# Performance work log

Measured on AMD Instinct MI355X. Metric: run time of the kernel, lower is better.

Reference implementation:

```python
import jax, jax.numpy as jnp
import numpy as np

ALPHA = 0.2  # LeakyReLU negative slope


def setup_inputs() -> dict:
    key = jax.random.key(0)
    k1, k2, k3 = jax.random.split(key, 3)
    B, N, F_in, F_out = 8, 2048, 256, 256
    h = jax.random.normal(k1, (B, N, F_in), dtype=jnp.float32)
    adj = jax.random.randint(k2, (B, N, N), 0, 2, dtype=jnp.int32)
    # xavier_uniform for W [F_in, F_out]
    limit = float(np.sqrt(6.0 / (F_in + F_out)))
    W = jax.random.uniform(k3, (F_in, F_out), dtype=jnp.float32, minval=-limit, maxval=limit)
    return {"h": h, "adj": adj, "W": W}


def reference(h, adj, W):
    # h: [B,N,F_in], W: [F_in,F_out] -> Wh: [B,N,F_out]
    Wh = jnp.einsum('bnf,fo->bno', h, W)
    # (Wh_i + Wh_j).sum(-1) == s[p] + s[q] with s = Wh.sum(-1); avoids [B,N,N,F] tensor
    s = Wh.sum(axis=-1)  # [B,N]
    e = jax.nn.leaky_relu(s[:, :, None] + s[:, None, :], negative_slope=ALPHA)  # [B,N,N]
    e = jnp.where(adj == 0, -jnp.inf, e)
    alpha = jax.nn.softmax(e, axis=-1)  # masked softmax over neighbors
    # dropout is identity in eval mode
    h_prime = jnp.einsum('bpq,bqo->bpo', alpha, Wh)  # [B,N,F_out]
    return h_prime
```

## Files before the change

kernel.cpp:

```cpp
#include <hip/hip_runtime.h>
#include <hip/hip_bf16.h>
#include <stdint.h>

#define LEAKY_ALPHA 0.2f

using f32x4 = __attribute__((ext_vector_type(4))) float;
using u32x2 = __attribute__((ext_vector_type(2))) unsigned int;
using u32x4 = __attribute__((ext_vector_type(4))) unsigned int;
using i32x4 = __attribute__((ext_vector_type(4))) int;
using s16x8 = __attribute__((ext_vector_type(8))) short;

static __device__ __forceinline__ unsigned short f2bf(float x) {
  __hip_bfloat16 b = __float2bfloat16(x);
  return __builtin_bit_cast(unsigned short, b);
}

__global__ __launch_bounds__(256) void gat_prep(
    const float* __restrict__ W, __hip_bfloat16* __restrict__ WT,
    float* __restrict__ wsum)
{
  const int o = blockIdx.x;
  const int t = threadIdx.x;
  WT[o * 256 + t] = __float2bfloat16(W[t * 256 + o]);
  float u = W[o * 256 + t];
#pragma unroll
  for (int off = 1; off < 64; off <<= 1) u += __shfl_xor(u, off, 64);
  __shared__ float red[4];
  if ((t & 63) == 0) red[t >> 6] = u;
  __syncthreads();
  if (t == 0) wsum[o] = red[0] + red[1] + red[2] + red[3];
}

__global__ __launch_bounds__(256) void gat_wh2(
    const float* __restrict__ h, const __hip_bfloat16* __restrict__ WT,
    const float* __restrict__ wsum, __hip_bfloat16* __restrict__ WhT,
    float* __restrict__ s)
{
  const int b = blockIdx.x >> 5;
  const int q0 = (blockIdx.x & 31) * 64;
  const int t = threadIdx.x;
  const int wid = t >> 6, lane = t & 63;

  __shared__ __align__(16) unsigned char Bh[64 * 512];
  __shared__ __align__(16) unsigned char Aw[256 * 128];
  __shared__ __align__(16) float wsl[256];

  wsl[t] = wsum[t];
  __syncthreads();

  {
    const int q = t >> 2;
    const int fs = (t & 3) * 64;
    const float* hrow = h + ((size_t)(b * 2048 + q0 + q)) * 256 + fs;
    float sp = 0.f;
#pragma unroll
    for (int c = 0; c < 8; ++c) {
      const f32x4 a  = *(const f32x4*)&hrow[c * 8];
      const f32x4 bq = *(const f32x4*)&hrow[c * 8 + 4];
      const f32x4 wa = *(const f32x4*)&wsl[fs + c * 8];
      const f32x4 wb = *(const f32x4*)&wsl[fs + c * 8 + 4];
      sp += a[0]*wa[0] + a[1]*wa[1] + a[2]*wa[2] + a[3]*wa[3]
          + bq[0]*wb[0] + bq[1]*wb[1] + bq[2]*wb[2] + bq[3]*wb[3];
      u32x4 pk;
      pk[0] = (unsigned)f2bf(a[0])  | ((unsigned)f2bf(a[1])  << 16);
      pk[1] = (unsigned)f2bf(a[2])  | ((unsigned)f2bf(a[3])  << 16);
      pk[2] = (unsigned)f2bf(bq[0]) | ((unsigned)f2bf(bq[1]) << 16);
      pk[3] = (unsigned)f2bf(bq[2]) | ((unsigned)f2bf(bq[3]) << 16);
      const int boff = q * 512 + ((fs * 2 + c * 16) ^ ((q & 7) << 4));
      *(u32x4*)&Bh[boff] = pk;
    }
    sp += __shfl_xor(sp, 1, 64);
    sp += __shfl_xor(sp, 2, 64);
    if ((t & 3) == 0) s[b * 2048 + q0 + q] = sp;
  }

  f32x4 acc[4][4];
#pragma unroll
  for (int i = 0; i < 4; ++i)
#pragma unroll
    for (int j = 0; j < 4; ++j) acc[i][j] = (f32x4)(0.f);

  for (int it = 0; it < 4; ++it) {
    const int f0 = it * 64;
    __syncthreads();
#pragma unroll
    for (int j = 0; j < 8; ++j) {
      const int o = (t >> 3) + 32 * j;
      const int c = t & 7;
      const u32x4 v = *(const u32x4*)&WT[o * 256 + f0 + c * 8];
      *(u32x4*)&Aw[o * 128 + ((c * 16) ^ ((o & 7) << 4))] = v;
    }
    __syncthreads();
#pragma unroll
    for (int kt = 0; kt < 2; ++kt) {
      const int kb = kt * 64 + ((lane >> 4) << 4);
      s16x8 af[4], bf[4];
#pragma unroll
      for (int qt = 0; qt < 4; ++qt) {
        const int qr = qt * 16 + (lane & 15);
        af[qt] = *(const s16x8*)&Bh[qr * 512 + ((f0 * 2 + kb) ^ ((qr & 7) << 4))];
      }
#pragma unroll
      for (int ot = 0; ot < 4; ++ot) {
        const int orow = wid * 64 + ot * 16 + (lane & 15);
        bf[ot] = *(const s16x8*)&Aw[orow * 128 + (kb ^ ((orow & 7) << 4))];
      }
#pragma unroll
      for (int qt = 0; qt < 4; ++qt)
#pragma unroll
        for (int ot = 0; ot < 4; ++ot)
          acc[qt][ot] = __builtin_amdgcn_mfma_f32_16x16x32_bf16(
              af[qt], bf[ot], acc[qt][ot], 0, 0, 0);
    }
  }

  __hip_bfloat16* __restrict__ WhTb = WhT + (size_t)b * 256 * 2048;
#pragma unroll
  for (int qt = 0; qt < 4; ++qt)
#pragma unroll
    for (int ot = 0; ot < 4; ++ot) {
      const int o = wid * 64 + ot * 16 + (lane & 15);
      const int ql = q0 + qt * 16 + ((lane >> 4) << 2);
      u32x2 pk;
      pk[0] = (unsigned)f2bf(acc[qt][ot][0]) | ((unsigned)f2bf(acc[qt][ot][1]) << 16);
      pk[1] = (unsigned)f2bf(acc[qt][ot][2]) | ((unsigned)f2bf(acc[qt][ot][3]) << 16);
      *(u32x2*)&WhTb[(size_t)o * 2048 + ql] = pk;
    }
}

__global__ __launch_bounds__(512, 2) void gat_attn(
    const int* __restrict__ adj, const float* __restrict__ s,
    const __hip_bfloat16* __restrict__ WhT, float* __restrict__ out)
{
  const int N = 2048;
  const int bid = blockIdx.x;
  const int swz = (bid & 7) * 32 + (bid >> 3);
  const int b = swz >> 5;
  const int p0 = (swz & 31) * 64;
  const int t = threadIdx.x;
  const int wid = t >> 6, lane = t & 63;

  __shared__ __align__(16) unsigned char Bs[2][256 * 128];
  __shared__ __align__(16) unsigned char Pt[2][64 * 128];
  __shared__ __align__(16) float red_sh[8];
  __shared__ __align__(16) float l_sh[64];

  const int sp_row = t >> 3;
  const int sq8 = (t & 7) * 8;
  const int* __restrict__ adjrow = adj + ((size_t)(b * N + p0 + sp_row)) * N;
  const float* __restrict__ sB = s + b * N;
  const __hip_bfloat16* __restrict__ WhTb = WhT + (size_t)b * 256 * 2048;
  const int ptoff = sp_row * 128 + (((t & 7) ^ (sp_row & 7)) << 4);

  const int grow = t >> 3;
  const int gchunk = t & 7;
  const size_t gsrc_off = (size_t)grow * 2048 + (size_t)((gchunk ^ (grow & 7)) << 3);
  const int ldst = wid * 1024;

  const int pg = wid >> 2;
  const int og = wid & 3;

#pragma unroll
  for (int c = 0; c < 4; ++c)
    __builtin_amdgcn_global_load_lds(
        (const __attribute__((address_space(1))) unsigned int*)(WhTb + gsrc_off + (size_t)c * 64 * 2048),
        (__attribute__((address_space(3))) unsigned int*)&Bs[0][c * 8192 + ldst],
        16, 0, 0);
  i32x4 aE0 = *(const i32x4*)&adjrow[sq8];
  i32x4 aE1 = *(const i32x4*)&adjrow[sq8 + 4];
  f32x4 sE0 = *(const f32x4*)&sB[sq8];
  f32x4 sE1 = *(const f32x4*)&sB[sq8 + 4];
  i32x4 aO0 = *(const i32x4*)&adjrow[64 + sq8];
  i32x4 aO1 = *(const i32x4*)&adjrow[64 + sq8 + 4];
  f32x4 sO0 = *(const f32x4*)&sB[64 + sq8];
  f32x4 sO1 = *(const f32x4*)&sB[64 + sq8 + 4];

  const f32x4 s4 = *(const f32x4*)&sB[t * 4];
  float bm = fmaxf(fmaxf(s4[0], s4[1]), fmaxf(s4[2], s4[3]));
#pragma unroll
  for (int off = 1; off < 64; off <<= 1) bm = fmaxf(bm, __shfl_xor(bm, off, 64));
  if (lane == 0) red_sh[wid] = bm;
  const float s_p = sB[p0 + sp_row];
  __syncthreads();
  float smax = red_sh[0];
#pragma unroll
  for (int k = 1; k < 8; ++k) smax = fmaxf(smax, red_sh[k]);
  const float xm = s_p + smax;
  const float m_p = (xm > 0.f) ? xm : (LEAKY_ALPHA * xm);

  f32x4 acc[2][4];
#pragma unroll
  for (int pt = 0; pt < 2; ++pt)
#pragma unroll
    for (int ot = 0; ot < 4; ++ot) acc[pt][ot] = (f32x4)(0.f);
  float lacc = 0.f;

  auto phase = [&](int BI, int QQ, i32x4& A0, i32x4& A1, f32x4& S0, f32x4& S1)
      __attribute__((always_inline)) {
    float wv[8];
#pragma unroll
    for (int i = 0; i < 4; ++i) {
      const float x = s_p + S0[i];
      const float le = (x > 0.f) ? x : (LEAKY_ALPHA * x);
      const float w = __expf(le - m_p);
      wv[i] = (A0[i] != 0) ? w : 0.f;
      lacc += wv[i];
    }
#pragma unroll
    for (int i = 0; i < 4; ++i) {
      const float x = s_p + S1[i];
      const float le = (x > 0.f) ? x : (LEAKY_ALPHA * x);
      const float w = __expf(le - m_p);
      wv[4 + i] = (A1[i] != 0) ? w : 0.f;
      lacc += wv[4 + i];
    }
    {
      u32x4 pw;
#pragma unroll
      for (int k2 = 0; k2 < 4; ++k2)
        pw[k2] = (unsigned)f2bf(wv[2 * k2]) |
                 ((unsigned)f2bf(wv[2 * k2 + 1]) << 16);
      *(u32x4*)&Pt[BI][ptoff] = pw;
    }
    {
      const int qr = (QQ + 128 < N) ? (QQ + 128) : (N - 64);
      A0 = *(const i32x4*)&adjrow[qr + sq8];
      A1 = *(const i32x4*)&adjrow[qr + sq8 + 4];
      S0 = *(const f32x4*)&sB[qr + sq8];
      S1 = *(const f32x4*)&sB[qr + sq8 + 4];
    }
    asm volatile("s_waitcnt vmcnt(4) lgkmcnt(0)" ::: "memory");
    __builtin_amdgcn_s_barrier();
    __builtin_amdgcn_sched_barrier(0);
    {
      const int qg = (QQ + 64 < N) ? (QQ + 64) : (N - 64);
      const __hip_bfloat16* gs = WhTb + qg + gsrc_off;
#pragma unroll
      for (int c = 0; c < 4; ++c)
        __builtin_amdgcn_global_load_lds(
            (const __attribute__((address_space(1))) unsigned int*)(gs + (size_t)c * 64 * 2048),
            (__attribute__((address_space(3))) unsigned int*)&Bs[BI ^ 1][c * 8192 + ldst],
            16, 0, 0);
    }
    {
      s16x8 afr[2][2], bfr[4][2];
#pragma unroll
      for (int pt = 0; pt < 2; ++pt)
#pragma unroll
        for (int kt = 0; kt < 2; ++kt) {
          const int pa = pg * 32 + pt * 16 + (lane & 15);
          const int ck = (kt * 4 + (lane >> 4)) ^ (pa & 7);
          afr[pt][kt] = *(const s16x8*)&Pt[BI][pa * 128 + ck * 16];
        }
#pragma unroll
      for (int ot = 0; ot < 4; ++ot)
#pragma unroll
        for (int kt = 0; kt < 2; ++kt) {
          const int ob = og * 64 + ot * 16 + (lane & 15);
          const int ck = (kt * 4 + (lane >> 4)) ^ (ob & 7);
          bfr[ot][kt] = *(const s16x8*)&Bs[BI][ob * 128 + ck * 16];
        }
#pragma unroll
      for (int pt = 0; pt < 2; ++pt)
#pragma unroll
        for (int ot = 0; ot < 4; ++ot)
#pragma unroll
          for (int kt = 0; kt < 2; ++kt)
            acc[pt][ot] = __builtin_amdgcn_mfma_f32_16x16x32_bf16(
                afr[pt][kt], bfr[ot][kt], acc[pt][ot], 0, 0, 0);
    }
  };

  for (int q0 = 0; q0 < N; q0 += 128) {
    phase(0, q0, aE0, aE1, sE0, sE1);
    phase(1, q0 + 64, aO0, aO1, sO0, sO1);
  }

  lacc += __shfl_xor(lacc, 1, 64);
  lacc += __shfl_xor(lacc, 2, 64);
  lacc += __shfl_xor(lacc, 4, 64);
  if ((t & 7) == 0) l_sh[sp_row] = lacc;
  __syncthreads();

#pragma unroll
  for (int pt = 0; pt < 2; ++pt) {
    const int pb = pg * 32 + pt * 16 + ((lane >> 4) << 2);
    const f32x4 lv = *(const f32x4*)&l_sh[pb];
    f32x4 inv;
#pragma unroll
    for (int r = 0; r < 4; ++r) inv[r] = 1.f / lv[r];
#pragma unroll
    for (int ot = 0; ot < 4; ++ot) {
      const int o = og * 64 + ot * 16 + (lane & 15);
#pragma unroll
      for (int r = 0; r < 4; ++r) {
        const int row = p0 + pb + r;
        out[((size_t)(b * N + row)) * 256 + o] = acc[pt][ot][r] * inv[r];
      }
    }
  }
}

extern "C" void kernel_launch(void* const* d_in, const int* in_sizes, int n_in,
                              void* d_out, int out_size, void* d_ws, size_t ws_size,
                              hipStream_t stream) {
  const float* h = (const float*)d_in[0];
  const int* adj = (const int*)d_in[1];
  const float* W = (const float*)d_in[2];
  float* out = (float*)d_out;

  char* ws = (char*)d_ws;
  __hip_bfloat16* WhT = (__hip_bfloat16*)ws;
  float* s = (float*)(ws + (size_t)8 * 1024 * 1024);
  __hip_bfloat16* WT = (__hip_bfloat16*)(ws + (size_t)8 * 1024 * 1024 + 65536);
  float* wsum = (float*)(ws + (size_t)8 * 1024 * 1024 + 65536 + 131072);

  gat_prep<<<256, 256, 0, stream>>>(W, WT, wsum);
  gat_wh2<<<256, 256, 0, stream>>>(h, WT, wsum, WhT, s);
  gat_attn<<<256, 512, 0, stream>>>(adj, s, WhT, out);
}
```

Measured before the change: 63.90 us.

## Split attention output features across two blocks and stage WhT through registers

The attention kernel now launches 512 blocks, each computing half of the 256 output features for a 64-row tile. This halves the shared B tile and accumulator count and raises the occupancy target to 4 blocks per CU. WhT tiles are loaded into registers and stored to LDS, replacing the direct global-to-LDS async loads. In exchange, every block recomputes the softmax weights and rereads the adjacency row, doubling adjacency traffic (the dominant byte stream). It also loses the asynchronous LDS load path.

Measured after the change: 60.07 us. 1.06x faster.

```diff
diff --git a/kernel.cpp b/kernel.cpp
--- a/kernel.cpp
+++ b/kernel.cpp
@@ -128,19 +128,21 @@
     }
 }
 
-__global__ __launch_bounds__(512, 2) void gat_attn(
+__global__ __launch_bounds__(512, 4) void gat_attn(
     const int* __restrict__ adj, const float* __restrict__ s,
     const __hip_bfloat16* __restrict__ WhT, float* __restrict__ out)
 {
   const int N = 2048;
   const int bid = blockIdx.x;
-  const int swz = (bid & 7) * 32 + (bid >> 3);
-  const int b = swz >> 5;
-  const int p0 = (swz & 31) * 64;
+  const int swz = (bid & 7) * 64 + (bid >> 3);
+  const int b = swz >> 6;
+  const int inner = swz & 63;
+  const int p0 = (inner >> 1) * 64;
+  const int o0 = (inner & 1) * 128;
   const int t = threadIdx.x;
   const int wid = t >> 6, lane = t & 63;
 
-  __shared__ __align__(16) unsigned char Bs[2][256 * 128];
+  __shared__ __align__(16) unsigned char Bs[2][128 * 128];
   __shared__ __align__(16) unsigned char Pt[2][64 * 128];
   __shared__ __align__(16) float red_sh[8];
   __shared__ __align__(16) float l_sh[64];
@@ -149,23 +151,20 @@
   const int sq8 = (t & 7) * 8;
   const int* __restrict__ adjrow = adj + ((size_t)(b * N + p0 + sp_row)) * N;
   const float* __restrict__ sB = s + b * N;
-  const __hip_bfloat16* __restrict__ WhTb = WhT + (size_t)b * 256 * 2048;
-  const int ptoff = sp_row * 128 + (((t & 7) ^ (sp_row & 7)) << 4);
-
-  const int grow = t >> 3;
-  const int gchunk = t & 7;
-  const size_t gsrc_off = (size_t)grow * 2048 + (size_t)((gchunk ^ (grow & 7)) << 3);
-  const int ldst = wid * 1024;
+  const __hip_bfloat16* __restrict__ WhTb =
+      WhT + (size_t)b * 256 * 2048 + (size_t)o0 * 2048;
+  const int ptoff = sp_row * 128 + (((t & 7) * 16) ^ ((sp_row & 7) << 4));
+
+  const int so = t >> 3;
+  const int q16 = t & 7;
 
   const int pg = wid >> 2;
   const int og = wid & 3;
 
-#pragma unroll
-  for (int c = 0; c < 4; ++c)
-    __builtin_amdgcn_global_load_lds(
-        (const __attribute__((address_space(1))) unsigned int*)(WhTb + gsrc_off + (size_t)c * 64 * 2048),
-        (__attribute__((address_space(3))) unsigned int*)&Bs[0][c * 8192 + ldst],
-        16, 0, 0);
+  u32x4 breg[2];
+#pragma unroll
+  for (int c = 0; c < 2; ++c)
+    breg[c] = *(const u32x4*)&WhTb[(size_t)(so + 64 * c) * 2048 + q16 * 8];
   i32x4 aE0 = *(const i32x4*)&adjrow[sq8];
   i32x4 aE1 = *(const i32x4*)&adjrow[sq8 + 4];
   f32x4 sE0 = *(const f32x4*)&sB[sq8];
@@ -188,11 +187,11 @@
   const float xm = s_p + smax;
   const float m_p = (xm > 0.f) ? xm : (LEAKY_ALPHA * xm);
 
-  f32x4 acc[2][4];
+  f32x4 acc[2][2];
 #pragma unroll
   for (int pt = 0; pt < 2; ++pt)
 #pragma unroll
-    for (int ot = 0; ot < 4; ++ot) acc[pt][ot] = (f32x4)(0.f);
+    for (int ot = 0; ot < 2; ++ot) acc[pt][ot] = (f32x4)(0.f);
   float lacc = 0.f;
 
   auto phase = [&](int BI, int QQ, i32x4& A0, i32x4& A1, f32x4& S0, f32x4& S1)
@@ -222,6 +221,17 @@
                  ((unsigned)f2bf(wv[2 * k2 + 1]) << 16);
       *(u32x4*)&Pt[BI][ptoff] = pw;
     }
+#pragma unroll
+    for (int c = 0; c < 2; ++c) {
+      const int o = so + 64 * c;
+      *(u32x4*)&Bs[BI][o * 128 + ((q16 * 16) ^ ((o & 7) << 4))] = breg[c];
+    }
+    if (QQ + 64 < N) {
+#pragma unroll
+      for (int c = 0; c < 2; ++c)
+        breg[c] = *(const u32x4*)&WhTb[(size_t)(so + 64 * c) * 2048 +
+                                       QQ + 64 + q16 * 8];
+    }
     {
       const int qr = (QQ + 128 < N) ? (QQ + 128) : (N - 64);
       A0 = *(const i32x4*)&adjrow[qr + sq8];
@@ -229,41 +239,31 @@
       S0 = *(const f32x4*)&sB[qr + sq8];
       S1 = *(const f32x4*)&sB[qr + sq8 + 4];
     }
-    asm volatile("s_waitcnt vmcnt(4) lgkmcnt(0)" ::: "memory");
+    asm volatile("s_waitcnt lgkmcnt(0)" ::: "memory");
     __builtin_amdgcn_s_barrier();
-    __builtin_amdgcn_sched_barrier(0);
+    asm volatile("" ::: "memory");
     {
-      const int qg = (QQ + 64 < N) ? (QQ + 64) : (N - 64);
-      const __hip_bfloat16* gs = WhTb + qg + gsrc_off;
-#pragma unroll
-      for (int c = 0; c < 4; ++c)
-        __builtin_amdgcn_global_load_lds(
-            (const __attribute__((address_space(1))) unsigned int*)(gs + (size_t)c * 64 * 2048),
-            (__attribute__((address_space(3))) unsigned int*)&Bs[BI ^ 1][c * 8192 + ldst],
-            16, 0, 0);
-    }
-    {
-      s16x8 afr[2][2], bfr[4][2];
+      s16x8 afr[2][2], bfr[2][2];
 #pragma unroll
       for (int pt = 0; pt < 2; ++pt)
 #pragma unroll
         for (int kt = 0; kt < 2; ++kt) {
           const int pa = pg * 32 + pt * 16 + (lane & 15);
-          const int ck = (kt * 4 + (lane >> 4)) ^ (pa & 7);
-          afr[pt][kt] = *(const s16x8*)&Pt[BI][pa * 128 + ck * 16];
+          const int kb = kt * 64 + ((lane >> 4) << 4);
+          afr[pt][kt] = *(const s16x8*)&Pt[BI][pa * 128 + (kb ^ ((pa & 7) << 4))];
         }
 #pragma unroll
-      for (int ot = 0; ot < 4; ++ot)
+      for (int ot = 0; ot < 2; ++ot)
 #pragma unroll
         for (int kt = 0; kt < 2; ++kt) {
-          const int ob = og * 64 + ot * 16 + (lane & 15);
-          const int ck = (kt * 4 + (lane >> 4)) ^ (ob & 7);
-          bfr[ot][kt] = *(const s16x8*)&Bs[BI][ob * 128 + ck * 16];
+          const int ob = og * 32 + ot * 16 + (lane & 15);
+          const int kb = kt * 64 + ((lane >> 4) << 4);
+          bfr[ot][kt] = *(const s16x8*)&Bs[BI][ob * 128 + (kb ^ ((ob & 7) << 4))];
         }
 #pragma unroll
       for (int pt = 0; pt < 2; ++pt)
 #pragma unroll
-        for (int ot = 0; ot < 4; ++ot)
+        for (int ot = 0; ot < 2; ++ot)
 #pragma unroll
           for (int kt = 0; kt < 2; ++kt)
             acc[pt][ot] = __builtin_amdgcn_mfma_f32_16x16x32_bf16(
@@ -290,8 +290,8 @@
 #pragma unroll
     for (int r = 0; r < 4; ++r) inv[r] = 1.f / lv[r];
 #pragma unroll
-    for (int ot = 0; ot < 4; ++ot) {
-      const int o = og * 64 + ot * 16 + (lane & 15);
+    for (int ot = 0; ot < 2; ++ot) {
+      const int o = o0 + og * 32 + ot * 16 + (lane & 15);
 #pragma unroll
       for (int r = 0; r < 4; ++r) {
         const int row = p0 + pb + r;
@@ -317,5 +317,5 @@
 
   gat_prep<<<256, 256, 0, stream>>>(W, WT, wsum);
   gat_wh2<<<256, 256, 0, stream>>>(h, WT, wsum, WhT, s);
-  gat_attn<<<256, 512, 0, stream>>>(adj, s, WhT, out);
-}
+  gat_attn<<<512, 512, 0, stream>>>(adj, s, WhT, out);
+}
```
